# Kernel tuning notes

Measured on AMD Instinct MI355X. Metric: run time of the kernel, lower is better.

The kernel has to match this reference:

```python
import jax, jax.numpy as jnp
import numpy as np

N = 16384      # number of points (pixels)
C = 64         # value channels of U
D_REF = 5      # bilateral reference feature dim (xy + rgb)


def setup_inputs() -> dict:
    key = jax.random.key(0)
    k1, k2 = jax.random.split(key)
    U = jax.random.normal(k1, (N, C), dtype=jnp.float32)
    ref = jax.random.normal(k2, (N, D_REF), dtype=jnp.float32)
    return {"U": U, "ref": ref}


def reference(U, ref):
    # Gaussian filtering on reference features (exact form of the LSH-approx filter):
    #   out[i] = sum_j exp(-0.5 * ||ref_i - ref_j||^2) * U[j]  -  U[i]
    sq = jnp.sum(ref * ref, axis=-1)                      # [N]
    d2 = sq[:, None] + sq[None, :] - 2.0 * (ref @ ref.T)  # [N, N] squared distances
    K = jnp.exp(-0.5 * jnp.maximum(d2, 0.0))              # [N, N] Gaussian kernel
    return K @ U - U                                       # [N, C]
```

## Files before the change

### kernel.cpp

```cpp
#include <hip/hip_runtime.h>
#include <hip/hip_bf16.h>
#include <stdint.h>

#define N_PTS 16384
#define C_CH  64
#define D_REF 5
#define LOG2E 1.44269504088896340736f
#define IBLOCKS 64

typedef __attribute__((ext_vector_type(8))) short bf16x8;
typedef __attribute__((ext_vector_type(4))) float f32x4;

__device__ __forceinline__ unsigned short bf16rn(float v) {
    unsigned u = __builtin_bit_cast(unsigned, v) + 0x8000u;
    return (unsigned short)(u >> 16);
}
__device__ __forceinline__ float bf16tof(unsigned x) {
    return __builtin_bit_cast(float, x << 16);
}
__device__ __forceinline__ unsigned pack2bf16(float lo, float hi) {
    unsigned a = __builtin_bit_cast(unsigned, lo) + 0x8000u;
    unsigned b = __builtin_bit_cast(unsigned, hi) + 0x8000u;
    return __builtin_amdgcn_perm(b, a, 0x07060302u);
}
__device__ __forceinline__ unsigned cvt2(float lo, float hi) {
#if __has_builtin(__builtin_amdgcn_cvt_pk_bf16_f32)
    typedef __attribute__((ext_vector_type(2))) __bf16 bf162_t;
    bf162_t r = __builtin_amdgcn_cvt_pk_bf16_f32(lo, hi);
    return __builtin_bit_cast(unsigned, r);
#else
    return pack2bf16(lo, hi);
#endif
}
__device__ __forceinline__ float fast_exp2(float x) {
#if __has_builtin(__builtin_amdgcn_exp2f)
    return __builtin_amdgcn_exp2f(x);
#else
    return exp2f(x);
#endif
}

__global__ __launch_bounds__(256) void prep_all(
    const float* __restrict__ U, const float* __restrict__ ref,
    unsigned short* __restrict__ packA, unsigned short* __restrict__ packB,
    unsigned short* __restrict__ utPack)
{
    const int bid = blockIdx.x;
    const int t   = threadIdx.x;

    if (bid < 512) {
        const int gid  = bid * 256 + t;
        const int half = gid >> 16;
        const int id   = gid & 0xFFFF;
        const int tile16 = id >> 6;
        const int lane = id & 63;
        const int q    = lane >> 4;
        const int m    = lane & 15;
        const int p = half ? (tile16 * 16 + m)
                           : ((tile16 >> 1) * 32 + (m >> 2) * 8 + (m & 3) + (tile16 & 1) * 4);

        const float* r = ref + (size_t)p * D_REF;
        float rv[5];
        float sq = 0.f;
#pragma unroll
        for (int d = 0; d < 5; ++d) { rv[d] = r[d]; sq += rv[d] * rv[d]; }
        const float h = -0.5f * LOG2E * sq;

        unsigned short bh[5], bl[5];
#pragma unroll
        for (int d = 0; d < 5; ++d) {
            const float base = half ? rv[d] * LOG2E : rv[d];
            bh[d] = bf16rn(base);
            bl[d] = bf16rn(base - bf16tof((unsigned)bh[d]));
        }
        const unsigned short hh  = bf16rn(h);
        const unsigned short hl  = bf16rn(h - bf16tof((unsigned)hh));
        const unsigned short one = 0x3F80;

        unsigned short outv[8];
#pragma unroll
        for (int tt = 0; tt < 8; ++tt) {
            const int k = q * 8 + tt;
            unsigned short v = 0;
            if (!half) {
                if      (k < 5)   v = bh[k];
                else if (k < 10)  v = bh[k - 5];
                else if (k < 15)  v = bl[k - 10];
                else if (k == 15) v = hh;
                else if (k == 16) v = hl;
                else if (k <= 18) v = one;
            } else {
                if      (k < 5)   v = bh[k];
                else if (k < 10)  v = bl[k - 5];
                else if (k < 15)  v = bh[k - 10];
                else if (k <= 16) v = one;
                else if (k == 17) v = hh;
                else if (k == 18) v = hl;
            }
            outv[tt] = v;
        }
        unsigned short* dst = (half ? packB : packA) + ((size_t)tile16 * 64 + lane) * 8;
        *(uint4*)dst = *(uint4*)outv;
    } else {
        const int b    = bid - 512;
        const int lane = t & 63;
        const int ct   = t >> 6;
        const int m    = lane & 15;
        const int q    = lane >> 4;
        const int c    = ct * 16 + m;
        const int jb   = b * 32 + q * 8;

        unsigned short outv[8];
#pragma unroll
        for (int e = 0; e < 8; ++e)
            outv[e] = bf16rn(U[(size_t)(jb + e) * C_CH + c]);
        *(uint4*)&utPack[(((size_t)b * 4 + ct) * 64 + lane) * 8] = *(uint4*)outv;
    }
}

template<int JS>
__global__ __launch_bounds__(256, 4) void lsh_main(
    const float* __restrict__ U,
    const unsigned short* __restrict__ packA,
    const unsigned short* __restrict__ packB,
    const unsigned short* __restrict__ utPack,
    unsigned short* __restrict__ part,
    float* __restrict__ out,
    int use_part)
{
    constexpr int JT = (N_PTS / JS) / 32;

    const int t    = threadIdx.x;
    const int lane = t & 63;
    const int wave = t >> 6;
    const int q    = lane >> 4;
    const int m    = lane & 15;

    const int ib = blockIdx.x / JS;
    const int js = blockIdx.x % JS;

    bf16x8 bfrag[4];
#pragma unroll
    for (int s = 0; s < 4; ++s) {
        const int itile = ib * 16 + wave * 4 + s;
        bfrag[s] = *(const bf16x8*)(packB + ((size_t)itile * 64 + lane) * 8);
    }

    f32x4 acc[4][4];
#pragma unroll
    for (int s = 0; s < 4; ++s)
#pragma unroll
        for (int ct = 0; ct < 4; ++ct) acc[s][ct] = (f32x4){0.f, 0.f, 0.f, 0.f};

    const unsigned short* baseA = packA  + (size_t)(js * JT) * 1024 + lane * 8;
    const unsigned short* baseU = utPack + (size_t)(js * JT) * 2048 + lane * 8;

#pragma unroll 2
    for (int jt = 0; jt < JT; ++jt) {
        const bf16x8 ga0 = *(const bf16x8*)(baseA + (size_t)jt * 1024);
        const bf16x8 ga1 = *(const bf16x8*)(baseA + (size_t)jt * 1024 + 512);

        const f32x4 z = (f32x4){0.f, 0.f, 0.f, 0.f};
        bf16x8 sfrag[4];
#pragma unroll
        for (int s = 0; s < 4; ++s) {
            const f32x4 g0 = __builtin_amdgcn_mfma_f32_16x16x32_bf16(ga0, bfrag[s], z, 0, 0, 0);
            const f32x4 g1 = __builtin_amdgcn_mfma_f32_16x16x32_bf16(ga1, bfrag[s], z, 0, 0, 0);
            union { unsigned u[4]; bf16x8 v; } sb;
            sb.u[0] = cvt2(fast_exp2(g0[0]), fast_exp2(g0[1]));
            sb.u[1] = cvt2(fast_exp2(g0[2]), fast_exp2(g0[3]));
            sb.u[2] = cvt2(fast_exp2(g1[0]), fast_exp2(g1[1]));
            sb.u[3] = cvt2(fast_exp2(g1[2]), fast_exp2(g1[3]));
            sfrag[s] = sb.v;
        }
#pragma unroll
        for (int ct = 0; ct < 4; ++ct) {
            const bf16x8 uf = *(const bf16x8*)(baseU + (size_t)jt * 2048 + ct * 512);
#pragma unroll
            for (int s = 0; s < 4; ++s)
                acc[s][ct] = __builtin_amdgcn_mfma_f32_16x16x32_bf16(
                    uf, sfrag[s], acc[s][ct], 0, 0, 0);
        }
    }

    if (use_part) {
        unsigned short* dst = part + ((size_t)ib * JS + js) * 16384;
#pragma unroll
        for (int s = 0; s < 4; ++s)
#pragma unroll
            for (int cp = 0; cp < 2; ++cp) {
                uint4 w;
                w.x = cvt2(acc[s][cp*2+0][0], acc[s][cp*2+0][1]);
                w.y = cvt2(acc[s][cp*2+0][2], acc[s][cp*2+0][3]);
                w.z = cvt2(acc[s][cp*2+1][0], acc[s][cp*2+1][1]);
                w.w = cvt2(acc[s][cp*2+1][2], acc[s][cp*2+1][3]);
                *(uint4*)(dst + ((s * 2 + cp) * 256 + t) * 8) = w;
            }
    } else {
#pragma unroll
        for (int s = 0; s < 4; ++s) {
            const int i_glob = ib * 256 + (wave * 4 + s) * 16 + m;
#pragma unroll
            for (int ct = 0; ct < 4; ++ct)
#pragma unroll
                for (int r2 = 0; r2 < 4; ++r2) {
                    const int c = ct * 16 + q * 4 + r2;
                    float val = acc[s][ct][r2];
                    if (js == 0) val -= U[(size_t)i_glob * C_CH + c];
                    atomicAdd(&out[(size_t)i_glob * C_CH + c], val);
                }
        }
    }
}

template<int JS>
__global__ __launch_bounds__(256) void reduce_part(
    const unsigned short* __restrict__ part, const float* __restrict__ U,
    float* __restrict__ out)
{
    const int ib   = blockIdx.x >> 3;
    const int s2cp = blockIdx.x & 7;
    const int tt   = threadIdx.x;
    const int s  = s2cp >> 1, cp = s2cp & 1;
    const int wv = tt >> 6, ln = tt & 63, q = ln >> 4, m = ln & 15;
    const int i  = ib * 256 + (wv * 4 + s) * 16 + m;

    float sums[8];
#pragma unroll
    for (int e = 0; e < 8; ++e) sums[e] = 0.f;

    const unsigned short* base =
        part + (size_t)ib * JS * 16384 + (size_t)(s2cp * 256 + tt) * 8;
#pragma unroll
    for (int js = 0; js < JS; ++js) {
        const uint4 w = *(const uint4*)(base + (size_t)js * 16384);
        sums[0] += bf16tof(w.x & 0xFFFFu); sums[1] += bf16tof(w.x >> 16);
        sums[2] += bf16tof(w.y & 0xFFFFu); sums[3] += bf16tof(w.y >> 16);
        sums[4] += bf16tof(w.z & 0xFFFFu); sums[5] += bf16tof(w.z >> 16);
        sums[6] += bf16tof(w.w & 0xFFFFu); sums[7] += bf16tof(w.w >> 16);
    }

#pragma unroll
    for (int cti = 0; cti < 2; ++cti) {
        const int c0 = (cp * 2 + cti) * 16 + q * 4;
        const f32x4 u = *(const f32x4*)(U + (size_t)i * 64 + c0);
        f32x4 r;
        r[0] = sums[cti * 4 + 0] - u[0];
        r[1] = sums[cti * 4 + 1] - u[1];
        r[2] = sums[cti * 4 + 2] - u[2];
        r[3] = sums[cti * 4 + 3] - u[3];
        *(f32x4*)(out + (size_t)i * 64 + c0) = r;
    }
}

extern "C" void kernel_launch(void* const* d_in, const int* in_sizes, int n_in,
                              void* d_out, int out_size, void* d_ws, size_t ws_size,
                              hipStream_t stream) {
    const float* U   = (const float*)d_in[0];
    const float* ref = (const float*)d_in[1];
    float* out = (float*)d_out;

    unsigned short* utPack = (unsigned short*)d_ws;
    unsigned short* packA  = (unsigned short*)((char*)d_ws + (size_t)2 * 1024 * 1024);
    unsigned short* packB  = (unsigned short*)((char*)d_ws + (size_t)3 * 1024 * 1024);
    unsigned short* part   = (unsigned short*)((char*)d_ws + (size_t)4 * 1024 * 1024);

    const size_t MB = 1024 * 1024;
    prep_all<<<1024, 256, 0, stream>>>(U, ref, packA, packB, utPack);

    if (ws_size >= 36 * MB) {
        lsh_main<16><<<IBLOCKS * 16, 256, 0, stream>>>(U, packA, packB, utPack,
                                                       part, out, 1);
        reduce_part<16><<<512, 256, 0, stream>>>(part, U, out);
    } else {
        hipMemsetAsync(d_out, 0, (size_t)out_size * sizeof(float), stream);
        lsh_main<8><<<IBLOCKS * 8, 256, 0, stream>>>(U, packA, packB, utPack,
                                                     part, out, 0);
    }
}
```

Measured before the change: 117.7 us.

## Fuse prep, main and reduce kernels into one cooperative launch with grid syncs

Merges the three kernels (packing, main Gaussian-filter MFMA loop, partial reduction) into a single cooperative kernel separated by grid-wide barriers, so there is one launch instead of three. If the cooperative launch fails it falls back to the separate kernels. The atomic/memset path for small workspaces is removed, so the fallback now assumes the large workspace is available. The fused kernel uses the 4-waves-per-SIMD launch bound for every phase, and grid syncs add barrier cost while requiring all 1024 blocks to be co-resident.

```diff
diff --git a/kernel.cpp b/kernel.cpp
--- a/kernel.cpp
+++ b/kernel.cpp
@@ -1,6 +1,9 @@
 #include <hip/hip_runtime.h>
 #include <hip/hip_bf16.h>
+#include <hip/hip_cooperative_groups.h>
 #include <stdint.h>
+
+namespace cg = cooperative_groups;
 
 #define N_PTS 16384
 #define C_CH  64
@@ -40,14 +43,12 @@
 #endif
 }
 
-__global__ __launch_bounds__(256) void prep_all(
+__device__ __forceinline__ void prep_work(
+    int bid, int t,
     const float* __restrict__ U, const float* __restrict__ ref,
     unsigned short* __restrict__ packA, unsigned short* __restrict__ packB,
     unsigned short* __restrict__ utPack)
 {
-    const int bid = blockIdx.x;
-    const int t   = threadIdx.x;
-
     if (bid < 512) {
         const int gid  = bid * 256 + t;
         const int half = gid >> 16;
@@ -119,25 +120,20 @@
 }
 
 template<int JS>
-__global__ __launch_bounds__(256, 4) void lsh_main(
-    const float* __restrict__ U,
+__device__ __forceinline__ void lsh_work(
+    int bid, int t,
     const unsigned short* __restrict__ packA,
     const unsigned short* __restrict__ packB,
     const unsigned short* __restrict__ utPack,
-    unsigned short* __restrict__ part,
-    float* __restrict__ out,
-    int use_part)
+    unsigned short* __restrict__ part)
 {
     constexpr int JT = (N_PTS / JS) / 32;
 
-    const int t    = threadIdx.x;
     const int lane = t & 63;
     const int wave = t >> 6;
-    const int q    = lane >> 4;
-    const int m    = lane & 15;
-
-    const int ib = blockIdx.x / JS;
-    const int js = blockIdx.x % JS;
+
+    const int ib = bid / JS;
+    const int js = bid % JS;
 
     bf16x8 bfrag[4];
 #pragma unroll
@@ -183,44 +179,28 @@
         }
     }
 
-    if (use_part) {
-        unsigned short* dst = part + ((size_t)ib * JS + js) * 16384;
-#pragma unroll
-        for (int s = 0; s < 4; ++s)
-#pragma unroll
-            for (int cp = 0; cp < 2; ++cp) {
-                uint4 w;
-                w.x = cvt2(acc[s][cp*2+0][0], acc[s][cp*2+0][1]);
-                w.y = cvt2(acc[s][cp*2+0][2], acc[s][cp*2+0][3]);
-                w.z = cvt2(acc[s][cp*2+1][0], acc[s][cp*2+1][1]);
-                w.w = cvt2(acc[s][cp*2+1][2], acc[s][cp*2+1][3]);
-                *(uint4*)(dst + ((s * 2 + cp) * 256 + t) * 8) = w;
-            }
-    } else {
-#pragma unroll
-        for (int s = 0; s < 4; ++s) {
-            const int i_glob = ib * 256 + (wave * 4 + s) * 16 + m;
-#pragma unroll
-            for (int ct = 0; ct < 4; ++ct)
-#pragma unroll
-                for (int r2 = 0; r2 < 4; ++r2) {
-                    const int c = ct * 16 + q * 4 + r2;
-                    float val = acc[s][ct][r2];
-                    if (js == 0) val -= U[(size_t)i_glob * C_CH + c];
-                    atomicAdd(&out[(size_t)i_glob * C_CH + c], val);
-                }
-        }
-    }
-}
-
-template<int JS>
-__global__ __launch_bounds__(256) void reduce_part(
+    unsigned short* dst = part + ((size_t)ib * JS + js) * 16384;
+#pragma unroll
+    for (int s = 0; s < 4; ++s)
+#pragma unroll
+        for (int cp = 0; cp < 2; ++cp) {
+            uint4 w;
+            w.x = cvt2(acc[s][cp*2+0][0], acc[s][cp*2+0][1]);
+            w.y = cvt2(acc[s][cp*2+0][2], acc[s][cp*2+0][3]);
+            w.z = cvt2(acc[s][cp*2+1][0], acc[s][cp*2+1][1]);
+            w.w = cvt2(acc[s][cp*2+1][2], acc[s][cp*2+1][3]);
+            *(uint4*)(dst + ((s * 2 + cp) * 256 + t) * 8) = w;
+        }
+}
+
+template<int JS>
+__device__ __forceinline__ void reduce_work(
+    int bid, int tt,
     const unsigned short* __restrict__ part, const float* __restrict__ U,
     float* __restrict__ out)
 {
-    const int ib   = blockIdx.x >> 3;
-    const int s2cp = blockIdx.x & 7;
-    const int tt   = threadIdx.x;
+    const int ib   = bid >> 3;
+    const int s2cp = bid & 7;
     const int s  = s2cp >> 1, cp = s2cp & 1;
     const int wv = tt >> 6, ln = tt & 63, q = ln >> 4, m = ln & 15;
     const int i  = ib * 256 + (wv * 4 + s) * 16 + m;
@@ -253,6 +233,49 @@
     }
 }
 
+template<int JS>
+__global__ __launch_bounds__(256, 4) void fused_all(
+    const float* __restrict__ U, const float* __restrict__ ref,
+    unsigned short* __restrict__ packA, unsigned short* __restrict__ packB,
+    unsigned short* __restrict__ utPack, unsigned short* __restrict__ part,
+    float* __restrict__ out)
+{
+    const int bid = blockIdx.x;
+    const int t   = threadIdx.x;
+
+    prep_work(bid, t, U, ref, packA, packB, utPack);
+    cg::this_grid().sync();
+    lsh_work<JS>(bid, t, packA, packB, utPack, part);
+    cg::this_grid().sync();
+    if (bid < 512) reduce_work<JS>(bid, t, part, U, out);
+}
+
+__global__ __launch_bounds__(256) void prep_all(
+    const float* __restrict__ U, const float* __restrict__ ref,
+    unsigned short* __restrict__ packA, unsigned short* __restrict__ packB,
+    unsigned short* __restrict__ utPack)
+{
+    prep_work(blockIdx.x, threadIdx.x, U, ref, packA, packB, utPack);
+}
+
+template<int JS>
+__global__ __launch_bounds__(256, 4) void lsh_main(
+    const unsigned short* __restrict__ packA,
+    const unsigned short* __restrict__ packB,
+    const unsigned short* __restrict__ utPack,
+    unsigned short* __restrict__ part)
+{
+    lsh_work<JS>(blockIdx.x, threadIdx.x, packA, packB, utPack, part);
+}
+
+template<int JS>
+__global__ __launch_bounds__(256) void reduce_part(
+    const unsigned short* __restrict__ part, const float* __restrict__ U,
+    float* __restrict__ out)
+{
+    reduce_work<JS>(blockIdx.x, threadIdx.x, part, U, out);
+}
+
 extern "C" void kernel_launch(void* const* d_in, const int* in_sizes, int n_in,
                               void* d_out, int out_size, void* d_ws, size_t ws_size,
                               hipStream_t stream) {
@@ -265,16 +288,18 @@
     unsigned short* packB  = (unsigned short*)((char*)d_ws + (size_t)3 * 1024 * 1024);
     unsigned short* part   = (unsigned short*)((char*)d_ws + (size_t)4 * 1024 * 1024);
 
-    const size_t MB = 1024 * 1024;
-    prep_all<<<1024, 256, 0, stream>>>(U, ref, packA, packB, utPack);
-
-    if (ws_size >= 36 * MB) {
-        lsh_main<16><<<IBLOCKS * 16, 256, 0, stream>>>(U, packA, packB, utPack,
-                                                       part, out, 1);
+    const float* pU = U; const float* pRef = ref;
+    unsigned short* pA = packA; unsigned short* pB = packB;
+    unsigned short* pUt = utPack; unsigned short* pPart = part;
+    float* pOut = out;
+    void* args[] = {&pU, &pRef, &pA, &pB, &pUt, &pPart, &pOut};
+
+    hipError_t err = hipLaunchCooperativeKernel(
+        fused_all<16>, dim3(1024), dim3(256), args, 0, stream);
+
+    if (err != hipSuccess) {
+        prep_all<<<1024, 256, 0, stream>>>(U, ref, packA, packB, utPack);
+        lsh_main<16><<<IBLOCKS * 16, 256, 0, stream>>>(packA, packB, utPack, part);
         reduce_part<16><<<512, 256, 0, stream>>>(part, U, out);
-    } else {
-        hipMemsetAsync(d_out, 0, (size_t)out_size * sizeof(float), stream);
-        lsh_main<8><<<IBLOCKS * 8, 256, 0, stream>>>(U, packA, packB, utPack,
-                                                     part, out, 0);
-    }
-}
+    }
+}
```

Result: slower. 385.3 us (+227.4%).
